# Performance work log

Hardware: AMD Instinct MI355X
Metric: run time of the kernel (lower is better)

The kernel has to match this reference:

```python
import jax, jax.numpy as jnp
import numpy as np

M0 = 0.01
R = 2.0

def setup_inputs() -> dict:
    key = jax.random.key(0)
    x = jax.random.uniform(key, (8, 1, 64, 64), dtype=jnp.float32)  # normalized images in [0,1)
    return {"x": x}

def reference(x):
    # Exact weighted DTM (the differentiable/GPU part of GudhiCubicalExtractor;
    # the subsequent GUDHI cubical persistence is a CPU library call, out of scope).
    B, C, H, W = x.shape
    N = H * W
    weights = x.reshape(B, N)  # [B, N]

    # pixel grid coordinates [N, 2]
    yy, xx = jnp.meshgrid(jnp.arange(H), jnp.arange(W), indexing='ij')
    coords = jnp.stack([yy.ravel(), xx.ravel()], axis=1).astype(jnp.float32)

    # pairwise Euclidean distances ^ r  -> [N, N]
    d2 = jnp.sum((coords[:, None, :] - coords[None, :, :]) ** 2, axis=-1)
    dists_pow = jnp.power(jnp.sqrt(d2), R)

    # sort distances per source pixel (batch-independent)
    order = jnp.argsort(dists_pow, axis=1)                      # [N, N]
    sorted_dists_pow = jnp.take_along_axis(dists_pow, order, axis=1)  # [N, N]

    # gather weights in sorted-distance order: [B, N, N]
    w_sorted = weights[:, order]

    total_mass = jnp.sum(weights, axis=1)       # [B]
    m_target = M0 * total_mass                  # [B]

    w_cumsum = jnp.cumsum(w_sorted, axis=2)
    prev_cumsum = w_cumsum - w_sorted
    remains = m_target[:, None, None] - prev_cumsum
    w_effective = jnp.clip(jnp.minimum(w_sorted, remains), 0.0)

    weighted_dist_sum = jnp.sum(w_effective * sorted_dists_pow[None], axis=2)  # [B, N]

    safe_m = jnp.where(m_target > 0, m_target, 1.0)
    dtm = jnp.power(weighted_dist_sum / safe_m[:, None], 1.0 / R)
    dtm = jnp.where((total_mass > 0)[:, None], dtm, 0.0)
    return dtm.reshape(B, H, W)
```

## Files before the change

### kernel.cpp

```cpp
#include <hip/hip_runtime.h>
#include <math.h>

#define BLOCK 128

namespace {
constexpr int Hh = 64;
constexpr int Ww = 64;
constexpr int NPIX = Hh * Ww;
constexpr int NBATCH = 8;
constexpr int NOFF = (2 * Hh - 1) * (2 * Ww - 1);
constexpr int D2MAX = (Hh - 1) * (Hh - 1) + (Ww - 1) * (Ww - 1);
constexpr int CHUNKS = NPIX / BLOCK;

struct OffTable { unsigned int v[NOFF]; };

constexpr OffTable make_table() {
  OffTable t{};
  int pos[D2MAX + 1] = {};
  for (int dy = -(Hh - 1); dy <= (Hh - 1); ++dy)
    for (int dx = -(Ww - 1); dx <= (Ww - 1); ++dx)
      pos[dy * dy + dx * dx] += 1;
  int acc = 0;
  for (int d = 0; d <= D2MAX; ++d) { int c = pos[d]; pos[d] = acc; acc += c; }
  for (int dy = -(Hh - 1); dy <= (Hh - 1); ++dy)
    for (int dx = -(Ww - 1); dx <= (Ww - 1); ++dx) {
      int d2 = dy * dy + dx * dx;
      t.v[pos[d2]++] = ((unsigned)d2 << 14) | ((unsigned)(dy + (Hh - 1)) << 7) |
                       (unsigned)(dx + (Ww - 1));
    }
  return t;
}
}

__device__ constexpr OffTable g_off = make_table();

__global__ __launch_bounds__(BLOCK) void dtm_kernel(const float* __restrict__ x,
                                                    float* __restrict__ out) {
  __shared__ __align__(16) float w[NPIX];
  __shared__ float wavesum[BLOCK / 64];

  const int b = blockIdx.x / CHUNKS;
  const int chunk = blockIdx.x % CHUNKS;
  const int tid = threadIdx.x;

  const float4* __restrict__ xb4 = (const float4*)(x + b * NPIX);
  float4* w4 = (float4*)w;
  float local = 0.f;
#pragma unroll
  for (int k = 0; k < NPIX / 4 / BLOCK; ++k) {
    float4 v = xb4[k * BLOCK + tid];
    w4[k * BLOCK + tid] = v;
    local += (v.x + v.y) + (v.z + v.w);
  }
#pragma unroll
  for (int off = 32; off > 0; off >>= 1) local += __shfl_xor(local, off);
  if ((tid & 63) == 0) wavesum[tid >> 6] = local;
  __syncthreads();
  float total = 0.f;
#pragma unroll
  for (int i = 0; i < BLOCK / 64; ++i) total += wavesum[i];
  const float T = 0.01f * total;

  const int pix = chunk * BLOCK + tid;
  const int py = pix >> 6;
  const int px = pix & 63;

  float cum = 0.f, wds = 0.f;
  for (int i = 0; i < NOFF; ++i) {
    const unsigned v = g_off.v[i];
    const int d2 = (int)(v >> 14);
    const int dy = (int)((v >> 7) & 127u) - (Hh - 1);
    const int dx = (int)(v & 127u) - (Ww - 1);
    const int ny = py + dy;
    const int nx = px + dx;
    if ((unsigned)ny < (unsigned)Hh && (unsigned)nx < (unsigned)Ww) {
      const float wv = w[ny * Ww + nx];
      float rem = T - cum;
      rem = rem > 0.f ? rem : 0.f;
      const float eff = wv < rem ? wv : rem;
      wds = fmaf(eff, (float)d2, wds);
      cum += wv;
    }
    if (__all(cum >= T)) break;
  }

  const float res = (T > 0.f) ? sqrtf(wds / T) : 0.f;
  out[b * NPIX + pix] = res;
}

extern "C" void kernel_launch(void* const* d_in, const int* in_sizes, int n_in,
                              void* d_out, int out_size, void* d_ws, size_t ws_size,
                              hipStream_t stream) {
  (void)in_sizes; (void)n_in; (void)out_size; (void)d_ws; (void)ws_size;
  const float* x = (const float*)d_in[0];
  float* out = (float*)d_out;
  dtm_kernel<<<dim3(NBATCH * CHUNKS), dim3(BLOCK), 0, stream>>>(x, out);
}
```

Before: 70.80 us.

## Pad LDS image, precompute offsets, and software-pipeline unrolled DTM loop

Stores the image in shared memory as a zero-padded 64x192 grid, so each neighbour becomes a single precomputed linear offset. This replaces the per-offset 2D bounds checks and the bit-unpacking of the packed table entry. The offset loop is unrolled by 8 and double-buffered, so table loads and shared-memory loads for the next group overlap the accumulation of the current one. The early-exit vote now runs once per group instead of per offset. In exchange, shared memory per block triples, which can lower occupancy, each block has to zero the padded buffer, and up to a group of extra offsets may be processed past the exit point.

Measured after the change: 59.08 us. -16.6%, faster.

```diff
diff --git a/kernel.cpp b/kernel.cpp
--- a/kernel.cpp
+++ b/kernel.cpp
@@ -2,87 +2,125 @@
 #include <math.h>
 
 #define BLOCK 128
+#define U 8
 
 namespace {
-constexpr int Hh = 64;
-constexpr int Ww = 64;
+constexpr int Hh = 64, Ww = 64;
 constexpr int NPIX = Hh * Ww;
 constexpr int NBATCH = 8;
-constexpr int NOFF = (2 * Hh - 1) * (2 * Ww - 1);
-constexpr int D2MAX = (Hh - 1) * (Hh - 1) + (Ww - 1) * (Ww - 1);
+constexpr int NOFF = 127 * 127;
+constexpr int D2MAX = 2 * 63 * 63;
 constexpr int CHUNKS = NPIX / BLOCK;
+constexpr int LW = 192;
+constexpr int LDSN = 64 * LW;
+constexpr int NMAIN = ((NOFF + 2 * U - 1) / (2 * U)) * (2 * U);
+constexpr int NOFFP = NMAIN + 2 * U;
 
-struct OffTable { unsigned int v[NOFF]; };
+struct Tab {
+  float d2f[NOFFP];
+  int rel[NOFFP];
+};
 
-constexpr OffTable make_table() {
-  OffTable t{};
+constexpr Tab make_table() {
+  Tab t{};
   int pos[D2MAX + 1] = {};
-  for (int dy = -(Hh - 1); dy <= (Hh - 1); ++dy)
-    for (int dx = -(Ww - 1); dx <= (Ww - 1); ++dx)
-      pos[dy * dy + dx * dx] += 1;
+  for (int dy = -63; dy <= 63; ++dy)
+    for (int dx = -63; dx <= 63; ++dx) pos[dy * dy + dx * dx] += 1;
   int acc = 0;
   for (int d = 0; d <= D2MAX; ++d) { int c = pos[d]; pos[d] = acc; acc += c; }
-  for (int dy = -(Hh - 1); dy <= (Hh - 1); ++dy)
-    for (int dx = -(Ww - 1); dx <= (Ww - 1); ++dx) {
-      int d2 = dy * dy + dx * dx;
-      t.v[pos[d2]++] = ((unsigned)d2 << 14) | ((unsigned)(dy + (Hh - 1)) << 7) |
-                       (unsigned)(dx + (Ww - 1));
+  for (int dy = -63; dy <= 63; ++dy)
+    for (int dx = -63; dx <= 63; ++dx) {
+      const int d2 = dy * dy + dx * dx;
+      const int p = pos[d2]++;
+      t.d2f[p] = (float)d2;
+      t.rel[p] = dy * LW + dx;
     }
+  for (int p = NOFF; p < NOFFP; ++p) { t.d2f[p] = 0.f; t.rel[p] = 4 * LDSN; }
   return t;
 }
 }
 
-__device__ constexpr OffTable g_off = make_table();
+__device__ constexpr Tab g_tab = make_table();
 
 __global__ __launch_bounds__(BLOCK) void dtm_kernel(const float* __restrict__ x,
                                                     float* __restrict__ out) {
-  __shared__ __align__(16) float w[NPIX];
+  __shared__ __align__(16) float w[LDSN];
   __shared__ float wavesum[BLOCK / 64];
 
   const int b = blockIdx.x / CHUNKS;
   const int chunk = blockIdx.x % CHUNKS;
   const int tid = threadIdx.x;
 
+  float4* w4 = (float4*)w;
+#pragma unroll
+  for (int k = 0; k < LDSN / 4 / BLOCK; ++k)
+    w4[k * BLOCK + tid] = float4{0.f, 0.f, 0.f, 0.f};
+  __syncthreads();
+
   const float4* __restrict__ xb4 = (const float4*)(x + b * NPIX);
-  float4* w4 = (float4*)w;
   float local = 0.f;
 #pragma unroll
   for (int k = 0; k < NPIX / 4 / BLOCK; ++k) {
-    float4 v = xb4[k * BLOCK + tid];
-    w4[k * BLOCK + tid] = v;
+    const int p4 = k * BLOCK + tid;
+    const float4 v = xb4[p4];
+    const int row = p4 >> 4;
+    const int col = (p4 & 15) << 2;
+    *(float4*)&w[row * LW + 64 + col] = v;
     local += (v.x + v.y) + (v.z + v.w);
   }
 #pragma unroll
-  for (int off = 32; off > 0; off >>= 1) local += __shfl_xor(local, off);
+  for (int off = 32; off; off >>= 1) local += __shfl_xor(local, off);
   if ((tid & 63) == 0) wavesum[tid >> 6] = local;
   __syncthreads();
-  float total = 0.f;
-#pragma unroll
-  for (int i = 0; i < BLOCK / 64; ++i) total += wavesum[i];
-  const float T = 0.01f * total;
+  const float T = 0.01f * (wavesum[0] + wavesum[1]);
 
   const int pix = chunk * BLOCK + tid;
-  const int py = pix >> 6;
-  const int px = pix & 63;
+  const int base = (pix >> 6) * LW + (pix & 63) + 64;
 
   float cum = 0.f, wds = 0.f;
-  for (int i = 0; i < NOFF; ++i) {
-    const unsigned v = g_off.v[i];
-    const int d2 = (int)(v >> 14);
-    const int dy = (int)((v >> 7) & 127u) - (Hh - 1);
-    const int dx = (int)(v & 127u) - (Ww - 1);
-    const int ny = py + dy;
-    const int nx = px + dx;
-    if ((unsigned)ny < (unsigned)Hh && (unsigned)nx < (unsigned)Ww) {
-      const float wv = w[ny * Ww + nx];
-      float rem = T - cum;
-      rem = rem > 0.f ? rem : 0.f;
-      const float eff = wv < rem ? wv : rem;
-      wds = fmaf(eff, (float)d2, wds);
-      cum += wv;
-    }
+  int relA[U], relB[U];
+  float d2A[U], d2B[U], wvA[U], wvB[U];
+
+#define TLOAD(BASE, REL, D2)                \
+  _Pragma("unroll") for (int u = 0; u < U; ++u) { \
+    REL[u] = g_tab.rel[(BASE) + u];         \
+    D2[u] = g_tab.d2f[(BASE) + u];          \
+  }
+
+#define WLOAD(REL, WV)                                                  \
+  _Pragma("unroll") for (int u = 0; u < U; ++u) {                       \
+    const int addr = base + REL[u];                                     \
+    const unsigned ac = min((unsigned)addr, (unsigned)(LDSN - 1));      \
+    const float val = w[ac];                                            \
+    WV[u] = ((unsigned)addr < (unsigned)LDSN) ? val : 0.f;              \
+  }
+
+#define ACC(WV, D2)                                \
+  _Pragma("unroll") for (int u = 0; u < U; ++u) {  \
+    float rem = T - cum;                           \
+    rem = rem > 0.f ? rem : 0.f;                   \
+    const float eff = WV[u] < rem ? WV[u] : rem;   \
+    wds = fmaf(eff, D2[u], wds);                   \
+    cum += WV[u];                                  \
+  }
+
+  TLOAD(0, relA, d2A);
+  WLOAD(relA, wvA);
+  TLOAD(U, relB, d2B);
+
+  for (int i = 0; i < NMAIN; i += 2 * U) {
+    WLOAD(relB, wvB);
+    ACC(wvA, d2A);
     if (__all(cum >= T)) break;
+    TLOAD(i + 2 * U, relA, d2A);
+    ACC(wvB, d2B);
+    if (__all(cum >= T)) break;
+    WLOAD(relA, wvA);
+    TLOAD(i + 3 * U, relB, d2B);
   }
+#undef TLOAD
+#undef WLOAD
+#undef ACC
 
   const float res = (T > 0.f) ? sqrtf(wds / T) : 0.f;
   out[b * NPIX + pix] = res;
```
